# Performance work log

Measured on AMD Instinct MI355X. Metric: run time of the kernel, lower is better.

Reference implementation:

```python
import jax, jax.numpy as jnp
import numpy as np


def _nn_idx(query, ref):
    """Index of nearest ref point for each query point.
    query: [B,N,3], ref: [B,M,3] -> idx [B,N] (int32).
    Squared distance via ||q||^2 - 2 q.r + ||r||^2 (matches cdist+top1).
    """
    d2 = (jnp.sum(query * query, axis=-1, keepdims=True)
          - 2.0 * jnp.einsum('bnd,bmd->bnm', query, ref)
          + jnp.sum(ref * ref, axis=-1)[:, None, :])
    return jnp.argmin(d2, axis=-1)


def setup_inputs() -> dict:
    key = jax.random.key(0)
    k1, k2, k3 = jax.random.split(key, 3)
    B, N, M = 1, 16384, 16384  # batch hard-coded to 1 in original loops
    pred = jax.random.normal(k1, (B, N, 3), dtype=jnp.float32)
    gt = jax.random.normal(k2, (B, M, 3), dtype=jnp.float32)
    weight = jax.random.uniform(k3, (1,), dtype=jnp.float32)
    return {"pred": pred, "gt": gt, "weight": weight}


def reference(pred, gt, weight):
    # get_mse_loss2: weighted bidirectional nearest-neighbor MSE.
    w = weight[0]
    # B2A: align each pred point to its nearest gt point
    idx = _nn_idx(pred, gt)                                   # [B,N]
    align_gt = jnp.take_along_axis(gt, idx[..., None], axis=1)  # [B,N,3]
    B2A = jnp.mean((pred - align_gt) ** 2)
    # A2B: align each gt point to its nearest pred point
    idx2 = _nn_idx(gt, pred)                                  # [B,M]
    align_out = jnp.take_along_axis(pred, idx2[..., None], axis=1)  # [B,M,3]
    A2B = jnp.mean((align_out - gt) ** 2)
    return B2A * w + A2B * (1.0 - w)
```

## Files before the change

### kernel.cpp

```cpp
#include <hip/hip_runtime.h>


#define NPTS   16384
#define QT     2
#define QBLK   (4 * QT * 32)
#define QCH    (NPTS / QBLK)
#define SSPLIT 16
#define RBLK   (NPTS / SSPLIT)
#define NB1    (2 * QCH * SSPLIT)

typedef __attribute__((ext_vector_type(8)))  __bf16 bf16x8;
typedef __attribute__((ext_vector_type(16))) float  floatx16;

union frag16 { __bf16 v[16]; uint4 q[2]; };

__device__ __forceinline__ float vmin16(floatx16 v) {
    float a = fminf(fminf(v[0], v[1]), v[2]);
    float b = fminf(fminf(v[3], v[4]), v[5]);
    float c = fminf(fminf(v[6], v[7]), v[8]);
    float d = fminf(fminf(v[9], v[10]), v[11]);
    float e = fminf(fminf(v[12], v[13]), fminf(v[14], v[15]));
    return fminf(fminf(fminf(a, b), fminf(c, d)), e);
}

__global__ __launch_bounds__(256) void prep_kernel(
    const float* __restrict__ pred, const float* __restrict__ gt,
    uint4* __restrict__ aform, uint4* __restrict__ bform,
    float* __restrict__ out)
{
    const int i = blockIdx.x * 256 + threadIdx.x;
    if (i == 0) out[0] = 0.0f;
    const int role = (i < NPTS) ? 0 : 1;
    const int p = i - role * NPTS;
    const float* __restrict__ src = role ? gt : pred;

    const float x = src[p * 3 + 0], y = src[p * 3 + 1], z = src[p * 3 + 2];
    const float nn = x * x + y * y + z * z;
    const __bf16 xh = (__bf16)x, yh = (__bf16)y, zh = (__bf16)z;
    const __bf16 xl = (__bf16)(x - (float)xh);
    const __bf16 yl = (__bf16)(y - (float)yh);
    const __bf16 zl = (__bf16)(z - (float)zh);
    const __bf16 nh = (__bf16)nn;
    const __bf16 nl = (__bf16)(nn - (float)nh);
    const __bf16 one = (__bf16)1.0f;

    frag16 A;
    A.v[0]  = (__bf16)(-2.0f * (float)xh); A.v[1]  = A.v[0];
    A.v[2]  = (__bf16)(-2.0f * (float)xl); A.v[3]  = A.v[2];
    A.v[4]  = (__bf16)(-2.0f * (float)yh); A.v[5]  = A.v[4];
    A.v[6]  = (__bf16)(-2.0f * (float)yl); A.v[7]  = A.v[6];
    A.v[8]  = (__bf16)(-2.0f * (float)zh); A.v[9]  = A.v[8];
    A.v[10] = (__bf16)(-2.0f * (float)zl); A.v[11] = A.v[10];
    A.v[12] = nh;  A.v[13] = nl;  A.v[14] = one;  A.v[15] = one;

    frag16 B;
    B.v[0] = xh;  B.v[1]  = xl;  B.v[2]  = xh;  B.v[3]  = xl;
    B.v[4] = yh;  B.v[5]  = yl;  B.v[6]  = yh;  B.v[7]  = yl;
    B.v[8] = zh;  B.v[9]  = zl;  B.v[10] = zh;  B.v[11] = zl;
    B.v[12] = one; B.v[13] = one; B.v[14] = nh;  B.v[15] = nl;

    uint4* da = aform + (size_t)role * (NPTS * 2)
              + ((p >> 5) * 64 + (p & 31));
    da[0]  = A.q[0];
    da[32] = A.q[1];
    uint4* db = bform + (size_t)role * (NPTS * 2) + p * 2;
    db[0] = B.q[0];
    db[1] = B.q[1];
}

__global__ __launch_bounds__(256) void nn_part_kernel(
    const uint4* __restrict__ aform, const uint4* __restrict__ bform,
    float* __restrict__ partial)
{
    const int bx   = blockIdx.x;
    const int dir  = bx >> 10;
    const int qc   = (bx & 1023) >> 4;
    const int s    = bx & 15;
    const int tid  = threadIdx.x;
    const int lane = tid & 63;
    const int wave = tid >> 6;
    const int lid  = lane & 31;
    const int half = lane >> 5;

    const uint4* __restrict__ Aref = aform + (size_t)(dir ? 0 : 1) * (NPTS * 2);
    const uint4* __restrict__ Bqry = bform + (size_t)(dir ? 1 : 0) * (NPTS * 2);

    const int qbase = qc * QBLK + wave * (QT * 32);
    bf16x8 bq[QT];
#pragma unroll
    for (int qt = 0; qt < QT; ++qt) {
        const int p = qbase + qt * 32 + lid;
        bq[qt] = __builtin_bit_cast(bf16x8, Bqry[p * 2 + half]);
    }

    floatx16 zero;
#pragma unroll
    for (int k = 0; k < 16; ++k) zero[k] = 0.0f;
    floatx16 mnv[QT];
#pragma unroll
    for (int qt = 0; qt < QT; ++qt)
#pragma unroll
        for (int k = 0; k < 16; ++k) mnv[qt][k] = 3.4e38f;

    const uint4* gp = Aref + (size_t)s * (RBLK * 2) + half * 32 + lid;
#pragma unroll 4
    for (int t = 0; t < RBLK / 32; t += 2) {
        const bf16x8 a0 = __builtin_bit_cast(bf16x8, gp[t * 64]);
        const bf16x8 a1 = __builtin_bit_cast(bf16x8, gp[t * 64 + 64]);
#pragma unroll
        for (int qt = 0; qt < QT; ++qt) {
            floatx16 d0 = __builtin_amdgcn_mfma_f32_32x32x16_bf16(a0, bq[qt], zero, 0, 0, 0);
            floatx16 d1 = __builtin_amdgcn_mfma_f32_32x32x16_bf16(a1, bq[qt], zero, 0, 0, 0);
#pragma unroll
            for (int k = 0; k < 16; ++k)
                mnv[qt][k] = fminf(fminf(mnv[qt][k], d0[k]), d1[k]);
        }
    }

    float* pout = partial + ((size_t)((dir * QCH + qc) * SSPLIT + s)) * QBLK
                + wave * (QT * 32);
#pragma unroll
    for (int qt = 0; qt < QT; ++qt) {
        float v = vmin16(mnv[qt]);
        v = fminf(v, __shfl_xor(v, 32));
        if (half == 0) pout[qt * 32 + lid] = v;
    }
}

__global__ __launch_bounds__(256) void nn_combine_kernel(
    const float* __restrict__ partial, const float* __restrict__ weight,
    float* __restrict__ out)
{
    const int b   = blockIdx.x;
    const int dir = b >> 6;
    const int qc  = b & 63;
    const int t   = threadIdx.x;

    const float* p = partial + ((size_t)((dir * QCH + qc) * SSPLIT)) * QBLK;
    float v = p[t];
#pragma unroll
    for (int s = 1; s < SSPLIT; ++s)
        v = fminf(v, p[s * QBLK + t]);

    for (int off = 32; off; off >>= 1) v += __shfl_down(v, off);
    __shared__ float ws[4];
    if ((t & 63) == 0) ws[t >> 6] = v;
    __syncthreads();
    if (t == 0) {
        const float sum = ws[0] + ws[1] + ws[2] + ws[3];
        const float wgt = weight[0];
        const float scale = (dir ? (1.0f - wgt) : wgt) / (3.0f * (float)NPTS);
        atomicAdd(out, sum * scale);
    }
}

extern "C" void kernel_launch(void* const* d_in, const int* in_sizes, int n_in,
                              void* d_out, int out_size, void* d_ws, size_t ws_size,
                              hipStream_t stream) {
    const float* pred   = (const float*)d_in[0];
    const float* gt     = (const float*)d_in[1];
    const float* weight = (const float*)d_in[2];

    float* partial = (float*)d_ws;
    uint4* aform = (uint4*)((char*)d_ws + (size_t)2 * QCH * SSPLIT * QBLK * 4);
    uint4* bform = aform + (size_t)2 * NPTS * 2;

    prep_kernel<<<2 * NPTS / 256, 256, 0, stream>>>(pred, gt, aform, bform,
                                                    (float*)d_out);
    nn_part_kernel<<<NB1, 256, 0, stream>>>(aform, bform, partial);
    nn_combine_kernel<<<2 * QCH, 256, 0, stream>>>(partial, weight, (float*)d_out);
}
```

Measured before the change: 85.01 us.

## Use one query tile per wave with hand-written inline-asm MFMA pairs

Each wave now handles a single 32-query tile instead of two, and the reference split drops from 16 to 8 chunks, so each block scans twice as many reference points. The two MFMAs per iteration are issued through inline asm followed by explicit s_nop padding to cover the result hazard, and the combine kernel shrinks to 128 threads. The aim is to cut register pressure and control instruction issue. In exchange, each loaded reference fragment is reused by half as many MFMAs, and the volatile asm with fixed nops stops the compiler from overlapping loads, MFMAs and min-reductions across iterations.

```diff
diff --git a/kernel.cpp b/kernel.cpp
--- a/kernel.cpp
+++ b/kernel.cpp
@@ -2,10 +2,9 @@
 
 
 #define NPTS   16384
-#define QT     2
-#define QBLK   (4 * QT * 32)
+#define QBLK   128
 #define QCH    (NPTS / QBLK)
-#define SSPLIT 16
+#define SSPLIT 8
 #define RBLK   (NPTS / SSPLIT)
 #define NB1    (2 * QCH * SSPLIT)
 
@@ -74,8 +73,8 @@
 {
     const int bx   = blockIdx.x;
     const int dir  = bx >> 10;
-    const int qc   = (bx & 1023) >> 4;
-    const int s    = bx & 15;
+    const int qc   = (bx & 1023) >> 3;
+    const int s    = bx & 7;
     const int tid  = threadIdx.x;
     const int lane = tid & 63;
     const int wave = tid >> 6;
@@ -85,55 +84,51 @@
     const uint4* __restrict__ Aref = aform + (size_t)(dir ? 0 : 1) * (NPTS * 2);
     const uint4* __restrict__ Bqry = bform + (size_t)(dir ? 1 : 0) * (NPTS * 2);
 
-    const int qbase = qc * QBLK + wave * (QT * 32);
-    bf16x8 bq[QT];
-#pragma unroll
-    for (int qt = 0; qt < QT; ++qt) {
-        const int p = qbase + qt * 32 + lid;
-        bq[qt] = __builtin_bit_cast(bf16x8, Bqry[p * 2 + half]);
-    }
+    const int qbase = qc * QBLK + wave * 32;
+    const bf16x8 bq = __builtin_bit_cast(bf16x8, Bqry[(qbase + lid) * 2 + half]);
 
     floatx16 zero;
 #pragma unroll
     for (int k = 0; k < 16; ++k) zero[k] = 0.0f;
-    floatx16 mnv[QT];
+    floatx16 mnv;
 #pragma unroll
-    for (int qt = 0; qt < QT; ++qt)
-#pragma unroll
-        for (int k = 0; k < 16; ++k) mnv[qt][k] = 3.4e38f;
+    for (int k = 0; k < 16; ++k) mnv[k] = 3.4e38f;
 
     const uint4* gp = Aref + (size_t)s * (RBLK * 2) + half * 32 + lid;
-#pragma unroll 4
+#pragma unroll 2
     for (int t = 0; t < RBLK / 32; t += 2) {
         const bf16x8 a0 = __builtin_bit_cast(bf16x8, gp[t * 64]);
         const bf16x8 a1 = __builtin_bit_cast(bf16x8, gp[t * 64 + 64]);
+        floatx16 d0, d1;
+        asm volatile(
+            "v_mfma_f32_32x32x16_bf16 %[D0], %[A0], %[B], %[Z]\n\t"
+            "v_mfma_f32_32x32x16_bf16 %[D1], %[A1], %[B], %[Z]\n\t"
+            "s_nop 7\n\t"
+            "s_nop 7\n\t"
+            "s_nop 7"
+            : [D0] "=&v"(d0), [D1] "=&v"(d1)
+            : [A0] "v"(a0), [A1] "v"(a1), [B] "v"(bq), [Z] "v"(zero));
 #pragma unroll
-        for (int qt = 0; qt < QT; ++qt) {
-            floatx16 d0 = __builtin_amdgcn_mfma_f32_32x32x16_bf16(a0, bq[qt], zero, 0, 0, 0);
-            floatx16 d1 = __builtin_amdgcn_mfma_f32_32x32x16_bf16(a1, bq[qt], zero, 0, 0, 0);
-#pragma unroll
-            for (int k = 0; k < 16; ++k)
-                mnv[qt][k] = fminf(fminf(mnv[qt][k], d0[k]), d1[k]);
-        }
+        for (int k = 0; k < 16; ++k)
+            mnv[k] = fminf(fminf(mnv[k], d0[k]), d1[k]);
     }
 
-    float* pout = partial + ((size_t)((dir * QCH + qc) * SSPLIT + s)) * QBLK
-                + wave * (QT * 32);
-#pragma unroll
-    for (int qt = 0; qt < QT; ++qt) {
-        float v = vmin16(mnv[qt]);
-        v = fminf(v, __shfl_xor(v, 32));
-        if (half == 0) pout[qt * 32 + lid] = v;
+    float v = vmin16(mnv);
+    v = fminf(v, __shfl_xor(v, 32));
+    if (half == 0) {
+        float* pout = partial + ((size_t)((dir * QCH + qc) * SSPLIT + s)) * QBLK
+                    + wave * 32;
+        pout[lid] = v;
     }
 }
 
-__global__ __launch_bounds__(256) void nn_combine_kernel(
+__global__ __launch_bounds__(QBLK) void nn_combine_kernel(
     const float* __restrict__ partial, const float* __restrict__ weight,
     float* __restrict__ out)
 {
     const int b   = blockIdx.x;
-    const int dir = b >> 6;
-    const int qc  = b & 63;
+    const int dir = b >> 7;
+    const int qc  = b & 127;
     const int t   = threadIdx.x;
 
     const float* p = partial + ((size_t)((dir * QCH + qc) * SSPLIT)) * QBLK;
@@ -143,11 +138,11 @@
         v = fminf(v, p[s * QBLK + t]);
 
     for (int off = 32; off; off >>= 1) v += __shfl_down(v, off);
-    __shared__ float ws[4];
+    __shared__ float ws[2];
     if ((t & 63) == 0) ws[t >> 6] = v;
     __syncthreads();
     if (t == 0) {
-        const float sum = ws[0] + ws[1] + ws[2] + ws[3];
+        const float sum = ws[0] + ws[1];
         const float wgt = weight[0];
         const float scale = (dir ? (1.0f - wgt) : wgt) / (3.0f * (float)NPTS);
         atomicAdd(out, sum * scale);
@@ -168,5 +163,5 @@
     prep_kernel<<<2 * NPTS / 256, 256, 0, stream>>>(pred, gt, aform, bform,
                                                     (float*)d_out);
     nn_part_kernel<<<NB1, 256, 0, stream>>>(aform, bform, partial);
-    nn_combine_kernel<<<2 * QCH, 256, 0, stream>>>(partial, weight, (float*)d_out);
+    nn_combine_kernel<<<2 * QCH, QBLK, 0, stream>>>(partial, weight, (float*)d_out);
 }
```

After: 87.47 us. 1.03x slower.
